# Kernel optimization log

Hardware: AMD Instinct MI355X
Metric: run time of the kernel (lower is better)

## Reference

```python
import jax, jax.numpy as jnp
import numpy as np
import math

D_MODEL = 1024
N_HEADS = 16
QKV_DIM = 1024
D_HEAD = QKV_DIM // N_HEADS


def setup_inputs() -> dict:
    key = jax.random.key(0)
    ks = jax.random.split(key, 10)
    B, S = 4, 2048
    lim = 1.0 / math.sqrt(D_MODEL)
    lim_o = 1.0 / math.sqrt(QKV_DIM)
    return {
        "x": jax.random.normal(ks[0], (B, S, D_MODEL), dtype=jnp.float32),
        "w_q": jax.random.uniform(ks[1], (QKV_DIM, D_MODEL), minval=-lim, maxval=lim, dtype=jnp.float32),
        "b_q": jax.random.uniform(ks[2], (QKV_DIM,), minval=-lim, maxval=lim, dtype=jnp.float32),
        "w_k": jax.random.uniform(ks[3], (QKV_DIM, D_MODEL), minval=-lim, maxval=lim, dtype=jnp.float32),
        "b_k": jax.random.uniform(ks[4], (QKV_DIM,), minval=-lim, maxval=lim, dtype=jnp.float32),
        "w_v": jax.random.uniform(ks[5], (QKV_DIM, D_MODEL), minval=-lim, maxval=lim, dtype=jnp.float32),
        "b_v": jax.random.uniform(ks[6], (QKV_DIM,), minval=-lim, maxval=lim, dtype=jnp.float32),
        "w_o": jax.random.uniform(ks[7], (D_MODEL, QKV_DIM), minval=-lim_o, maxval=lim_o, dtype=jnp.float32),
        "b_o": jax.random.uniform(ks[8], (D_MODEL,), minval=-lim_o, maxval=lim_o, dtype=jnp.float32),
        "temperature": jnp.ones((1,), dtype=jnp.float32),
        "q_scale": jnp.ones((N_HEADS,), dtype=jnp.float32),
    }


def reference(x, w_q, b_q, w_k, b_k, w_v, b_v, w_o, b_o, temperature, q_scale):
    B, S, _ = x.shape
    # QKV projections: [B,S,qkv_dim] -> [B,H,S,Dh]
    def proj(w, b):
        y = jnp.einsum('bsd,ed->bse', x, w) + b
        return y.reshape(B, S, N_HEADS, D_HEAD).transpose(0, 2, 1, 3)
    q = proj(w_q, b_q)
    k = proj(w_k, b_k)
    v = proj(w_v, b_v)
    scale = jnp.sqrt(jnp.float32(D_HEAD)) * temperature[0]
    scores = jnp.einsum('bhqd,bhkd->bhqk', q, k) / scale
    attn = jax.nn.softmax(scores, axis=-1)
    attn = attn * q_scale.reshape(1, N_HEADS, 1, 1)  # per-head post-softmax scale
    out = jnp.einsum('bhqk,bhkd->bhqd', attn, v)
    out = out.transpose(0, 2, 1, 3).reshape(B, S, QKV_DIM)
    return jnp.einsum('bse,de->bsd', out, w_o) + b_o
```

## Files before the change

### kernel.cpp

```cpp
#include <hip/hip_runtime.h>
#include <hip/hip_bf16.h>
#include <stdint.h>

typedef __bf16 bf16;
typedef __bf16 bf16x8 __attribute__((ext_vector_type(8)));
typedef __bf16 bf16x4 __attribute__((ext_vector_type(4)));
typedef float f32x4 __attribute__((ext_vector_type(4)));
typedef float f32x16 __attribute__((ext_vector_type(16)));

#define NB 4
#define SEQ 2048
#define DM 1024
#define NHEADS 16
#define DHEAD 64
#define MTOK (NB*SEQ)
#define NE 3072

__device__ __forceinline__ void gl_lds16(const bf16* g, bf16* l) {
  __builtin_amdgcn_global_load_lds(
      (const __attribute__((address_space(1))) void*)g,
      (__attribute__((address_space(3))) void*)l, 16, 0, 0);
}

__device__ __forceinline__ f32x16 zero16() {
  f32x16 z;
#pragma unroll
  for (int i=0;i<16;i++) z[i]=0.f;
  return z;
}

__global__ __launch_bounds__(256) void convert_kernel(
    const float* __restrict__ x,
    const float* __restrict__ wq, const float* __restrict__ wk,
    const float* __restrict__ wv, const float* __restrict__ wo,
    const float* __restrict__ bq, const float* __restrict__ bk,
    const float* __restrict__ bv,
    bf16* __restrict__ xb, bf16* __restrict__ wqkvb,
    bf16* __restrict__ wob, float* __restrict__ bqkv) {
  int tid = blockIdx.x*blockDim.x + threadIdx.x;
  int nt = gridDim.x*blockDim.x;
  const int NX4 = MTOK*DM/4;
  for (int i = tid; i < NX4; i += nt) {
    float4 v = ((const float4*)x)[i];
    ((bf16x4*)xb)[i] = bf16x4{(bf16)v.x,(bf16)v.y,(bf16)v.z,(bf16)v.w};
  }
  const int NW4 = DM*DM/4;
  for (int i = tid; i < NW4; i += nt) {
    float4 a = ((const float4*)wq)[i];
    ((bf16x4*)wqkvb)[i] = bf16x4{(bf16)a.x,(bf16)a.y,(bf16)a.z,(bf16)a.w};
    float4 b = ((const float4*)wk)[i];
    ((bf16x4*)wqkvb)[i+NW4] = bf16x4{(bf16)b.x,(bf16)b.y,(bf16)b.z,(bf16)b.w};
    float4 c = ((const float4*)wv)[i];
    ((bf16x4*)wqkvb)[i+2*NW4] = bf16x4{(bf16)c.x,(bf16)c.y,(bf16)c.z,(bf16)c.w};
    float4 d = ((const float4*)wo)[i];
    ((bf16x4*)wob)[i] = bf16x4{(bf16)d.x,(bf16)d.y,(bf16)d.z,(bf16)d.w};
  }
  for (int i = tid; i < DM; i += nt) {
    bqkv[i] = bq[i]; bqkv[i+DM] = bk[i]; bqkv[i+2*DM] = bv[i];
  }
}

template<int OUT_MODE>
__global__ __launch_bounds__(256) void gemm_deep(
    const bf16* __restrict__ A, const bf16* __restrict__ Bm,
    const float* __restrict__ bias, void* __restrict__ Cout,
    int M, int N, int K) {
  __shared__ bf16 As[2][128*64];
  __shared__ bf16 Bs[2][128*64];
  const int bm = blockIdx.x, bn = blockIdx.y;
  const int thr = threadIdx.x;
  const int w = thr>>6, lane = thr&63;
  const int wr = w>>1, wc = w&1;
  const int l4 = lane>>4, lm = lane&15;
  f32x4 acc[4][4];
#pragma unroll
  for (int m=0;m<4;m++)
#pragma unroll
    for (int n=0;n<4;n++) acc[m][n] = f32x4{0.f,0.f,0.f,0.f};

  const bf16* Abase = A + (size_t)bm*128*K;
  const bf16* Bbase = Bm + (size_t)bn*128*K;

  const int srow = thr>>3;
  const int sch  = ((thr&7) ^ (srow&7)) * 8;
  const bf16* Ag = Abase + (size_t)srow*K + sch;
  const bf16* Bg = Bbase + (size_t)srow*K + sch;
  const int dbase = thr*8;

  const int nk = K>>6;

  int aoff[2][4], boff[2][4];
#pragma unroll
  for (int ks=0;ks<2;ks++) {
#pragma unroll
    for (int m=0;m<4;m++) {
      const int r = wr*64 + m*16 + lm;
      aoff[ks][m] = r*64 + ((((ks<<2)|l4) ^ (lm&7))*8);
    }
#pragma unroll
    for (int n=0;n<4;n++) {
      const int r = wc*64 + n*16 + lm;
      boff[ks][n] = r*64 + ((((ks<<2)|l4) ^ (lm&7))*8);
    }
  }

#pragma unroll
  for (int c=0;c<4;c++) {
    gl_lds16(Ag + (size_t)c*32*K, &As[0][c*2048 + dbase]);
    gl_lds16(Bg + (size_t)c*32*K, &Bs[0][c*2048 + dbase]);
  }

  for (int kt=0; kt<nk; ++kt) {
    const int p = kt&1;
    const int st = (kt+1 < nk) ? kt+1 : 0;
    const size_t ko = (size_t)st*64;
#pragma unroll
    for (int c=0;c<4;c++) {
      gl_lds16(Ag + ko + (size_t)c*32*K, &As[p^1][c*2048 + dbase]);
      gl_lds16(Bg + ko + (size_t)c*32*K, &Bs[p^1][c*2048 + dbase]);
    }
    asm volatile("s_waitcnt vmcnt(8)" ::: "memory");
    __builtin_amdgcn_s_barrier();
    __builtin_amdgcn_sched_barrier(0);

    const bf16* Ac = As[p];
    const bf16* Bc = Bs[p];
    __builtin_amdgcn_s_setprio(1);
#pragma unroll
    for (int ks=0;ks<2;ks++) {
      bf16x8 af[4], bfr[4];
#pragma unroll
      for (int m=0;m<4;m++) af[m] = *(const bf16x8*)&Ac[aoff[ks][m]];
#pragma unroll
      for (int n=0;n<4;n++) bfr[n] = *(const bf16x8*)&Bc[boff[ks][n]];
#pragma unroll
      for (int m=0;m<4;m++)
#pragma unroll
        for (int n=0;n<4;n++)
          acc[m][n] = __builtin_amdgcn_mfma_f32_16x16x32_bf16(af[m], bfr[n], acc[m][n], 0, 0, 0);
    }
    __builtin_amdgcn_s_setprio(0);
    __builtin_amdgcn_s_barrier();
    __builtin_amdgcn_sched_barrier(0);
  }

  const int rbase = bm*128 + wr*64 + l4*4;
  const int cbase = bn*128 + wc*64;
#pragma unroll
  for (int n=0;n<4;n++) {
    const int col = cbase + n*16 + lm;
    const float bv = bias[col];
#pragma unroll
    for (int m=0;m<4;m++) {
#pragma unroll
      for (int j=0;j<4;j++) {
        const int row = rbase + m*16 + j;
        const float v = acc[m][n][j] + bv;
        if (OUT_MODE == 0) ((bf16*)Cout)[(size_t)row*N + col] = (bf16)v;
        else               ((float*)Cout)[(size_t)row*N + col] = v;
      }
    }
  }
}

__global__ __launch_bounds__(256) void transpose_v(const bf16* __restrict__ qkv,
                                                   bf16* __restrict__ vt) {
  __shared__ bf16 tile[64*72];
  const int s0 = blockIdx.x*64;
  const int bh = blockIdx.y;
  const bf16* src = qkv + (size_t)((bh>>4)*SEQ + s0)*NE + 2*DM + (bh&15)*64;
  const int thr = threadIdx.x;
#pragma unroll
  for (int i=0;i<2;i++) {
    int idx = thr + i*256;
    int row = idx>>3, part = idx&7;
    *(bf16x8*)&tile[row*72 + part*8] = *(const bf16x8*)(src + (size_t)row*NE + part*8);
  }
  __syncthreads();
  bf16* dst = vt + (size_t)bh*64*SEQ + s0;
#pragma unroll
  for (int i=0;i<2;i++) {
    int idx = thr + i*256;
    int d = idx>>3, part = idx&7;
    bf16x8 v;
#pragma unroll
    for (int j=0;j<8;j++) v[j] = tile[(part*8+j)*72 + d];
    *(bf16x8*)(dst + (size_t)d*SEQ + part*8) = v;
  }
}

__global__ __launch_bounds__(256) void attn_kernel(
    const bf16* __restrict__ qkv, const bf16* __restrict__ vt,
    bf16* __restrict__ aout,
    const float* __restrict__ temperature, const float* __restrict__ q_scale) {
  __shared__ bf16 smem[4][64*64];
  const int bh = blockIdx.y;
  const int b = bh>>4, h = bh&15;
  const int thr = threadIdx.x;
  const int w = thr>>6, lane = thr&63;
  const int l31 = lane&31, hi = lane>>5;
  const float sc2 = 1.4426950408889634f / (8.0f * temperature[0]);
  const int q0 = blockIdx.x*128 + w*32;
  const int NT = SEQ/64;
#define KBUFB 8192
#define VOFFB 16384

  bf16x8 qf[4];
  {
    const bf16* qp = qkv + (size_t)(b*SEQ + q0 + l31)*NE + h*64 + hi*8;
#pragma unroll
    for (int s=0;s<4;s++) {
      bf16x8 qr = *(const bf16x8*)(qp + s*16);
#pragma unroll
      for (int j=0;j<8;j++) qf[s][j] = (bf16)((float)qr[j] * sc2);
    }
  }

  f32x16 o0 = zero16(), o1 = zero16(), l_acc = zero16();
  const bf16 onev = (bf16)1.0f;
  const bf16x8 ones = {onev,onev,onev,onev,onev,onev,onev,onev};

  const bf16* Kbase = qkv + (size_t)b*SEQ*NE + DM + h*64;
  const bf16* Vbase = vt + (size_t)bh*64*SEQ;

  const int sr = thr>>2, scb = thr&3;
  const int wb0 = sr*128 + (((scb*2+0) ^ (sr&7))<<4);
  const int wb1 = sr*128 + (((scb*2+1) ^ (sr&7))<<4);
  const int rsw = l31&7;

  const char* kr0[4];
  const char* kr1[4];
#pragma unroll
  for (int s=0;s<4;s++) {
    const int slot = s*2 + hi;
    kr0[s] = (const char*)smem + l31*128      + ((slot ^ rsw)<<4);
    kr1[s] = (const char*)smem + (32+l31)*128 + ((slot ^ rsw)<<4);
  }

  const bf16* kgb = Kbase + (size_t)sr*NE + scb*16;
  const bf16* vgb = Vbase + (size_t)sr*SEQ + scb*16;

  bf16x8 ka, kb, va, vb;
  ka = *(const bf16x8*)(kgb);
  kb = *(const bf16x8*)(kgb + 8);
  va = *(const bf16x8*)(vgb);
  vb = *(const bf16x8*)(vgb + 8);
  *(bf16x8*)((char*)smem + wb0)         = ka;
  *(bf16x8*)((char*)smem + wb1)         = kb;
  *(bf16x8*)((char*)smem + VOFFB + wb0) = va;
  *(bf16x8*)((char*)smem + VOFFB + wb1) = vb;
  kgb += (size_t)64*NE; vgb += 64;
  ka = *(const bf16x8*)(kgb);
  kb = *(const bf16x8*)(kgb + 8);
  va = *(const bf16x8*)(vgb);
  vb = *(const bf16x8*)(vgb + 8);
  kgb += (size_t)64*NE; vgb += 64;
  __syncthreads();

#define ATTN_TILE(P, T)                                                        \
  {                                                                            \
    const int t_ = (T);                                                        \
    if (t_ < NT-1) {                                                           \
      *(bf16x8*)((char*)smem + ((P)^1)*KBUFB + wb0)         = ka;              \
      *(bf16x8*)((char*)smem + ((P)^1)*KBUFB + wb1)         = kb;              \
      *(bf16x8*)((char*)smem + VOFFB + ((P)^1)*KBUFB + wb0) = va;              \
      *(bf16x8*)((char*)smem + VOFFB + ((P)^1)*KBUFB + wb1) = vb;              \
      if (t_ < NT-2) {                                                         \
        ka = *(const bf16x8*)(kgb);                                            \
        kb = *(const bf16x8*)(kgb + 8);                                        \
        va = *(const bf16x8*)(vgb);                                            \
        vb = *(const bf16x8*)(vgb + 8);                                        \
        kgb += (size_t)64*NE; vgb += 64;                                       \
      }                                                                        \
    }                                                                          \
    f32x16 st0 = zero16(), st1 = zero16();                                     \
    __builtin_amdgcn_s_setprio(1);                                             \
    _Pragma("unroll")                                                          \
    for (int s=0;s<4;s++) {                                                    \
      bf16x8 kf0 = *(const bf16x8*)(kr0[s] + (P)*KBUFB);                       \
      bf16x8 kf1 = *(const bf16x8*)(kr1[s] + (P)*KBUFB);                       \
      st0 = __builtin_amdgcn_mfma_f32_32x32x16_bf16(kf0, qf[s], st0, 0,0,0);   \
      st1 = __builtin_amdgcn_mfma_f32_32x32x16_bf16(kf1, qf[s], st1, 0,0,0);   \
    }                                                                          \
    __builtin_amdgcn_s_setprio(0);                                             \
    _Pragma("unroll")                                                          \
    for (int r=0;r<16;r++) st0[r] = __builtin_amdgcn_exp2f(st0[r]);            \
    _Pragma("unroll")                                                          \
    for (int r=0;r<16;r++) st1[r] = __builtin_amdgcn_exp2f(st1[r]);            \
    __builtin_amdgcn_s_setprio(1);                                             \
    _Pragma("unroll")                                                          \
    for (int ks=0;ks<4;ks++) {                                                 \
      float e0,e1,e2,e3,e4,e5,e6,e7;                                           \
      if (ks==0)      { e0=st0[0]; e1=st0[1]; e2=st0[2]; e3=st0[3];            \
                        e4=st0[4]; e5=st0[5]; e6=st0[6]; e7=st0[7]; }          \
      else if (ks==1) { e0=st0[8]; e1=st0[9]; e2=st0[10];e3=st0[11];           \
                        e4=st0[12];e5=st0[13];e6=st0[14];e7=st0[15]; }         \
      else if (ks==2) { e0=st1[0]; e1=st1[1]; e2=st1[2]; e3=st1[3];            \
                        e4=st1[4]; e5=st1[5]; e6=st1[6]; e7=st1[7]; }          \
      else            { e0=st1[8]; e1=st1[9]; e2=st1[10];e3=st1[11];           \
                        e4=st1[12];e5=st1[13];e6=st1[14];e7=st1[15]; }         \
      unsigned a0,a1,b0,b1;                                                    \
      asm("v_cvt_pk_bf16_f32 %0, %1, %2" : "=v"(a0) : "v"(e0), "v"(e1));       \
      asm("v_cvt_pk_bf16_f32 %0, %1, %2" : "=v"(a1) : "v"(e2), "v"(e3));       \
      asm("v_cvt_pk_bf16_f32 %0, %1, %2" : "=v"(b0) : "v"(e4), "v"(e5));       \
      asm("v_cvt_pk_bf16_f32 %0, %1, %2" : "=v"(b1) : "v"(e6), "v"(e7));       \
      asm("v_permlane32_swap_b32 %0, %1" : "+v"(a0), "+v"(b0));                \
      asm("v_permlane32_swap_b32 %0, %1" : "+v"(a1), "+v"(b1));                \
      union { unsigned u[4]; bf16x8 v; } pu;                                   \
      pu.u[0]=a0; pu.u[1]=a1; pu.u[2]=b0; pu.u[3]=b1;                          \
      bf16x8 vf0, vf1;                                                         \
      if (ks==0) { vf0 = *(const bf16x8*)(kr0[0] + VOFFB + (P)*KBUFB);         \
                   vf1 = *(const bf16x8*)(kr1[0] + VOFFB + (P)*KBUFB); }       \
      else if (ks==1) { vf0 = *(const bf16x8*)(kr0[1] + VOFFB + (P)*KBUFB);    \
                   vf1 = *(const bf16x8*)(kr1[1] + VOFFB + (P)*KBUFB); }       \
      else if (ks==2) { vf0 = *(const bf16x8*)(kr0[2] + VOFFB + (P)*KBUFB);    \
                   vf1 = *(const bf16x8*)(kr1[2] + VOFFB + (P)*KBUFB); }       \
      else { vf0 = *(const bf16x8*)(kr0[3] + VOFFB + (P)*KBUFB);               \
             vf1 = *(const bf16x8*)(kr1[3] + VOFFB + (P)*KBUFB); }             \
      o0 = __builtin_amdgcn_mfma_f32_32x32x16_bf16(pu.v, vf0, o0, 0,0,0);      \
      o1 = __builtin_amdgcn_mfma_f32_32x32x16_bf16(pu.v, vf1, o1, 0,0,0);      \
      l_acc = __builtin_amdgcn_mfma_f32_32x32x16_bf16(pu.v, ones, l_acc, 0,0,0); \
    }                                                                          \
    __builtin_amdgcn_s_setprio(0);                                             \
    __syncthreads();                                                           \
  }

  for (int t2=0; t2<NT/2; ++t2) {
    ATTN_TILE(0, 2*t2);
    ATTN_TILE(1, 2*t2+1);
  }
#undef ATTN_TILE

  const float qs = q_scale[h];
#pragma unroll
  for (int r=0;r<16;r++) {
    const int qi = (r&3) + 8*(r>>2) + hi*4;
    const float iv = qs / l_acc[r];
    bf16* op = aout + (size_t)(b*SEQ + q0 + qi)*DM + h*64 + l31;
    op[0]  = (bf16)(o0[r]*iv);
    op[32] = (bf16)(o1[r]*iv);
  }
}

extern "C" void kernel_launch(void* const* d_in, const int* in_sizes, int n_in,
                              void* d_out, int out_size, void* d_ws, size_t ws_size,
                              hipStream_t stream) {
  (void)in_sizes; (void)n_in; (void)out_size; (void)ws_size;
  const float* x  = (const float*)d_in[0];
  const float* wq = (const float*)d_in[1];
  const float* bq = (const float*)d_in[2];
  const float* wk = (const float*)d_in[3];
  const float* bk = (const float*)d_in[4];
  const float* wv = (const float*)d_in[5];
  const float* bv = (const float*)d_in[6];
  const float* wo = (const float*)d_in[7];
  const float* bo = (const float*)d_in[8];
  const float* temp = (const float*)d_in[9];
  const float* qsc  = (const float*)d_in[10];

  char* ws = (char*)d_ws;
  bf16* xb    = (bf16*)ws; ws += (size_t)MTOK*DM*2;
  bf16* wqkvb = (bf16*)ws; ws += (size_t)NE*DM*2;
  bf16* wob   = (bf16*)ws; ws += (size_t)DM*DM*2;
  float* bqkv = (float*)ws; ws += (size_t)NE*4;
  bf16* qkv   = (bf16*)ws; ws += (size_t)MTOK*NE*2;
  bf16* vt    = (bf16*)ws; ws += (size_t)NB*NHEADS*DHEAD*SEQ*2;
  bf16* aout  = (bf16*)ws; ws += (size_t)MTOK*DM*2;

  convert_kernel<<<dim3(1024), dim3(256), 0, stream>>>(x, wq, wk, wv, wo, bq, bk, bv,
                                                       xb, wqkvb, wob, bqkv);
  gemm_deep<0><<<dim3(MTOK/128, NE/128), dim3(256), 0, stream>>>(xb, wqkvb, bqkv, qkv,
                                                                 MTOK, NE, DM);
  transpose_v<<<dim3(SEQ/64, NB*NHEADS), dim3(256), 0, stream>>>(qkv, vt);
  attn_kernel<<<dim3(SEQ/128, NB*NHEADS), dim3(256), 0, stream>>>(qkv, vt, aout, temp, qsc);
  gemm_deep<1><<<dim3(MTOK/128, DM/128), dim3(256), 0, stream>>>(aout, wob, bo, d_out,
                                                                 MTOK, DM, DM);
}
```

Before: 195.9 us.

## Process two 32-query sub-tiles per wave in attention to reuse K/V fragments

```diff
diff --git a/kernel.cpp b/kernel.cpp
--- a/kernel.cpp
+++ b/kernel.cpp
@@ -189,7 +189,7 @@
   }
 }
 
-__global__ __launch_bounds__(256) void attn_kernel(
+__global__ __launch_bounds__(256, 2) void attn_kernel(
     const bf16* __restrict__ qkv, const bf16* __restrict__ vt,
     bf16* __restrict__ aout,
     const float* __restrict__ temperature, const float* __restrict__ q_scale) {
@@ -200,23 +200,29 @@
   const int w = thr>>6, lane = thr&63;
   const int l31 = lane&31, hi = lane>>5;
   const float sc2 = 1.4426950408889634f / (8.0f * temperature[0]);
-  const int q0 = blockIdx.x*128 + w*32;
+  const int q0 = blockIdx.x*256 + w*64;
   const int NT = SEQ/64;
 #define KBUFB 8192
 #define VOFFB 16384
 
-  bf16x8 qf[4];
+  bf16x8 qfA[4], qfB[4];
   {
-    const bf16* qp = qkv + (size_t)(b*SEQ + q0 + l31)*NE + h*64 + hi*8;
+    const bf16* qpA = qkv + (size_t)(b*SEQ + q0 + l31)*NE + h*64 + hi*8;
+    const bf16* qpB = qpA + (size_t)32*NE;
 #pragma unroll
     for (int s=0;s<4;s++) {
-      bf16x8 qr = *(const bf16x8*)(qp + s*16);
-#pragma unroll
-      for (int j=0;j<8;j++) qf[s][j] = (bf16)((float)qr[j] * sc2);
-    }
-  }
-
-  f32x16 o0 = zero16(), o1 = zero16(), l_acc = zero16();
+      bf16x8 qa = *(const bf16x8*)(qpA + s*16);
+      bf16x8 qb = *(const bf16x8*)(qpB + s*16);
+#pragma unroll
+      for (int j=0;j<8;j++) {
+        qfA[s][j] = (bf16)((float)qa[j] * sc2);
+        qfB[s][j] = (bf16)((float)qb[j] * sc2);
+      }
+    }
+  }
+
+  f32x16 oA0 = zero16(), oA1 = zero16(), lA = zero16();
+  f32x16 oB0 = zero16(), oB1 = zero16(), lB = zero16();
   const bf16 onev = (bf16)1.0f;
   const bf16x8 ones = {onev,onev,onev,onev,onev,onev,onev,onev};
 
@@ -257,6 +263,25 @@
   kgb += (size_t)64*NE; vgb += 64;
   __syncthreads();
 
+#define MAKE_PU(PU, S0, S1, KS)                                                \
+  { float e0,e1,e2,e3,e4,e5,e6,e7;                                             \
+    if ((KS)==0)      { e0=S0[0]; e1=S0[1]; e2=S0[2]; e3=S0[3];                \
+                        e4=S0[4]; e5=S0[5]; e6=S0[6]; e7=S0[7]; }              \
+    else if ((KS)==1) { e0=S0[8]; e1=S0[9]; e2=S0[10];e3=S0[11];               \
+                        e4=S0[12];e5=S0[13];e6=S0[14];e7=S0[15]; }             \
+    else if ((KS)==2) { e0=S1[0]; e1=S1[1]; e2=S1[2]; e3=S1[3];                \
+                        e4=S1[4]; e5=S1[5]; e6=S1[6]; e7=S1[7]; }              \
+    else              { e0=S1[8]; e1=S1[9]; e2=S1[10];e3=S1[11];               \
+                        e4=S1[12];e5=S1[13];e6=S1[14];e7=S1[15]; }             \
+    unsigned a0,a1,b0,b1;                                                      \
+    asm("v_cvt_pk_bf16_f32 %0, %1, %2" : "=v"(a0) : "v"(e0), "v"(e1));         \
+    asm("v_cvt_pk_bf16_f32 %0, %1, %2" : "=v"(a1) : "v"(e2), "v"(e3));         \
+    asm("v_cvt_pk_bf16_f32 %0, %1, %2" : "=v"(b0) : "v"(e4), "v"(e5));         \
+    asm("v_cvt_pk_bf16_f32 %0, %1, %2" : "=v"(b1) : "v"(e6), "v"(e7));         \
+    asm("v_permlane32_swap_b32 %0, %1" : "+v"(a0), "+v"(b0));                  \
+    asm("v_permlane32_swap_b32 %0, %1" : "+v"(a1), "+v"(b1));                  \
+    PU.u[0]=a0; PU.u[1]=a1; PU.u[2]=b0; PU.u[3]=b1; }
+
 #define ATTN_TILE(P, T)                                                        \
   {                                                                            \
     const int t_ = (T);                                                        \
@@ -273,41 +298,32 @@
         kgb += (size_t)64*NE; vgb += 64;                                       \
       }                                                                        \
     }                                                                          \
-    f32x16 st0 = zero16(), st1 = zero16();                                     \
+    f32x16 sA0 = zero16(), sA1 = zero16(), sB0 = zero16(), sB1 = zero16();     \
     __builtin_amdgcn_s_setprio(1);                                             \
     _Pragma("unroll")                                                          \
     for (int s=0;s<4;s++) {                                                    \
       bf16x8 kf0 = *(const bf16x8*)(kr0[s] + (P)*KBUFB);                       \
       bf16x8 kf1 = *(const bf16x8*)(kr1[s] + (P)*KBUFB);                       \
-      st0 = __builtin_amdgcn_mfma_f32_32x32x16_bf16(kf0, qf[s], st0, 0,0,0);   \
-      st1 = __builtin_amdgcn_mfma_f32_32x32x16_bf16(kf1, qf[s], st1, 0,0,0);   \
+      sA0 = __builtin_amdgcn_mfma_f32_32x32x16_bf16(kf0, qfA[s], sA0, 0,0,0);  \
+      sB0 = __builtin_amdgcn_mfma_f32_32x32x16_bf16(kf0, qfB[s], sB0, 0,0,0);  \
+      sA1 = __builtin_amdgcn_mfma_f32_32x32x16_bf16(kf1, qfA[s], sA1, 0,0,0);  \
+      sB1 = __builtin_amdgcn_mfma_f32_32x32x16_bf16(kf1, qfB[s], sB1, 0,0,0);  \
     }                                                                          \
     __builtin_amdgcn_s_setprio(0);                                             \
     _Pragma("unroll")                                                          \
-    for (int r=0;r<16;r++) st0[r] = __builtin_amdgcn_exp2f(st0[r]);            \
-    _Pragma("unroll")                                                          \
-    for (int r=0;r<16;r++) st1[r] = __builtin_amdgcn_exp2f(st1[r]);            \
+    for (int r=0;r<16;r++) sA0[r] = __builtin_amdgcn_exp2f(sA0[r]);            \
+    _Pragma("unroll")                                                          \
+    for (int r=0;r<16;r++) sA1[r] = __builtin_amdgcn_exp2f(sA1[r]);            \
+    _Pragma("unroll")                                                          \
+    for (int r=0;r<16;r++) sB0[r] = __builtin_amdgcn_exp2f(sB0[r]);            \
+    _Pragma("unroll")                                                          \
+    for (int r=0;r<16;r++) sB1[r] = __builtin_amdgcn_exp2f(sB1[r]);            \
     __builtin_amdgcn_s_setprio(1);                                             \
     _Pragma("unroll")                                                          \
     for (int ks=0;ks<4;ks++) {                                                 \
-      float e0,e1,e2,e3,e4,e5,e6,e7;                                           \
-      if (ks==0)      { e0=st0[0]; e1=st0[1]; e2=st0[2]; e3=st0[3];            \
-                        e4=st0[4]; e5=st0[5]; e6=st0[6]; e7=st0[7]; }          \
-      else if (ks==1) { e0=st0[8]; e1=st0[9]; e2=st0[10];e3=st0[11];           \
-                        e4=st0[12];e5=st0[13];e6=st0[14];e7=st0[15]; }         \
-      else if (ks==2) { e0=st1[0]; e1=st1[1]; e2=st1[2]; e3=st1[3];            \
-                        e4=st1[4]; e5=st1[5]; e6=st1[6]; e7=st1[7]; }          \
-      else            { e0=st1[8]; e1=st1[9]; e2=st1[10];e3=st1[11];           \
-                        e4=st1[12];e5=st1[13];e6=st1[14];e7=st1[15]; }         \
-      unsigned a0,a1,b0,b1;                                                    \
-      asm("v_cvt_pk_bf16_f32 %0, %1, %2" : "=v"(a0) : "v"(e0), "v"(e1));       \
-      asm("v_cvt_pk_bf16_f32 %0, %1, %2" : "=v"(a1) : "v"(e2), "v"(e3));       \
-      asm("v_cvt_pk_bf16_f32 %0, %1, %2" : "=v"(b0) : "v"(e4), "v"(e5));       \
-      asm("v_cvt_pk_bf16_f32 %0, %1, %2" : "=v"(b1) : "v"(e6), "v"(e7));       \
-      asm("v_permlane32_swap_b32 %0, %1" : "+v"(a0), "+v"(b0));                \
-      asm("v_permlane32_swap_b32 %0, %1" : "+v"(a1), "+v"(b1));                \
-      union { unsigned u[4]; bf16x8 v; } pu;                                   \
-      pu.u[0]=a0; pu.u[1]=a1; pu.u[2]=b0; pu.u[3]=b1;                          \
+      union { unsigned u[4]; bf16x8 v; } puA, puB;                             \
+      MAKE_PU(puA, sA0, sA1, ks);                                              \
+      MAKE_PU(puB, sB0, sB1, ks);                                              \
       bf16x8 vf0, vf1;                                                         \
       if (ks==0) { vf0 = *(const bf16x8*)(kr0[0] + VOFFB + (P)*KBUFB);         \
                    vf1 = *(const bf16x8*)(kr1[0] + VOFFB + (P)*KBUFB); }       \
@@ -317,9 +333,12 @@
                    vf1 = *(const bf16x8*)(kr1[2] + VOFFB + (P)*KBUFB); }       \
       else { vf0 = *(const bf16x8*)(kr0[3] + VOFFB + (P)*KBUFB);               \
              vf1 = *(const bf16x8*)(kr1[3] + VOFFB + (P)*KBUFB); }             \
-      o0 = __builtin_amdgcn_mfma_f32_32x32x16_bf16(pu.v, vf0, o0, 0,0,0);      \
-      o1 = __builtin_amdgcn_mfma_f32_32x32x16_bf16(pu.v, vf1, o1, 0,0,0);      \
-      l_acc = __builtin_amdgcn_mfma_f32_32x32x16_bf16(pu.v, ones, l_acc, 0,0,0); \
+      oA0 = __builtin_amdgcn_mfma_f32_32x32x16_bf16(puA.v, vf0, oA0, 0,0,0);   \
+      oA1 = __builtin_amdgcn_mfma_f32_32x32x16_bf16(puA.v, vf1, oA1, 0,0,0);   \
+      lA  = __builtin_amdgcn_mfma_f32_32x32x16_bf16(puA.v, ones, lA, 0,0,0);   \
+      oB0 = __builtin_amdgcn_mfma_f32_32x32x16_bf16(puB.v, vf0, oB0, 0,0,0);   \
+      oB1 = __builtin_amdgcn_mfma_f32_32x32x16_bf16(puB.v, vf1, oB1, 0,0,0);   \
+      lB  = __builtin_amdgcn_mfma_f32_32x32x16_bf16(puB.v, ones, lB, 0,0,0);   \
     }                                                                          \
     __builtin_amdgcn_s_setprio(0);                                             \
     __syncthreads();                                                           \
@@ -330,15 +349,24 @@
     ATTN_TILE(1, 2*t2+1);
   }
 #undef ATTN_TILE
+#undef MAKE_PU
 
   const float qs = q_scale[h];
 #pragma unroll
   for (int r=0;r<16;r++) {
     const int qi = (r&3) + 8*(r>>2) + hi*4;
-    const float iv = qs / l_acc[r];
-    bf16* op = aout + (size_t)(b*SEQ + q0 + qi)*DM + h*64 + l31;
-    op[0]  = (bf16)(o0[r]*iv);
-    op[32] = (bf16)(o1[r]*iv);
+    {
+      const float iv = qs / lA[r];
+      bf16* op = aout + (size_t)(b*SEQ + q0 + qi)*DM + h*64 + l31;
+      op[0]  = (bf16)(oA0[r]*iv);
+      op[32] = (bf16)(oA1[r]*iv);
+    }
+    {
+      const float iv = qs / lB[r];
+      bf16* op = aout + (size_t)(b*SEQ + q0 + 32 + qi)*DM + h*64 + l31;
+      op[0]  = (bf16)(oB0[r]*iv);
+      op[32] = (bf16)(oB1[r]*iv);
+    }
   }
 }
 
@@ -372,7 +400,7 @@
   gemm_deep<0><<<dim3(MTOK/128, NE/128), dim3(256), 0, stream>>>(xb, wqkvb, bqkv, qkv,
                                                                  MTOK, NE, DM);
   transpose_v<<<dim3(SEQ/64, NB*NHEADS), dim3(256), 0, stream>>>(qkv, vt);
-  attn_kernel<<<dim3(SEQ/128, NB*NHEADS), dim3(256), 0, stream>>>(qkv, vt, aout, temp, qsc);
+  attn_kernel<<<dim3(SEQ/256, NB*NHEADS), dim3(256), 0, stream>>>(qkv, vt, aout, temp, qsc);
   gemm_deep<1><<<dim3(MTOK/128, DM/128), dim3(256), 0, stream>>>(aout, wob, bo, d_out,
                                                                  MTOK, DM, DM);
 }
```

Measured after the change: 181.3 us (median of 2 runs). 1.08x faster.
